# Performance work log

Measured on AMD Instinct MI355X. Metric: run time of the kernel, lower is better.

## Reference

```python
import math
import jax, jax.numpy as jnp
import numpy as np

H = 8      # num_heads
K = 3      # polynomial order
WH, WW = 8, 8  # win_size


def _relative_position_index(wh, ww):
    coords = np.stack(np.meshgrid(np.arange(wh), np.arange(ww), indexing='ij'))  # [2,wh,ww]
    cf = coords.reshape(2, -1)                       # [2, N]
    rel = cf[:, :, None] - cf[:, None, :]            # [2, N, N]
    rel = rel.transpose(1, 2, 0).astype(np.int64)    # [N, N, 2]
    rel[..., 0] += wh - 1
    rel[..., 1] += ww - 1
    rel[..., 0] *= 2 * ww - 1
    return rel.sum(-1)                               # [N, N]


def setup_inputs() -> dict:
    key = jax.random.key(0)
    ks = jax.random.split(key, 10)
    B, N, C = 1024, WH * WW, 256
    hd = C // H
    s = 0.02
    inp = {
        'x': jax.random.normal(ks[0], (B, N, C), dtype=jnp.float32),
        'Wq': jax.random.normal(ks[1], (C, C), dtype=jnp.float32) * s,
        'bq': jnp.zeros((C,), dtype=jnp.float32),
        'Wkv': jax.random.normal(ks[2], (C, 2 * C), dtype=jnp.float32) * s,
        'bkv': jnp.zeros((2 * C,), dtype=jnp.float32),
        'Wgate': jax.random.normal(ks[3], (hd, K + 1), dtype=jnp.float32) * s,
        'bgate': jnp.zeros((K + 1,), dtype=jnp.float32),
        'Wproj': jax.random.normal(ks[4], (C, C), dtype=jnp.float32) * s,
        'bproj': jnp.zeros((C,), dtype=jnp.float32),
        'bias_table': jax.random.normal(ks[5], ((2 * WH - 1) * (2 * WW - 1), H), dtype=jnp.float32) * s,
        'rel_index': jnp.asarray(_relative_position_index(WH, WW)),
    }
    return inp


def reference(x, Wq, bq, Wkv, bkv, Wgate, bgate, Wproj, bproj, bias_table, rel_index):
    B, N, C = x.shape
    hd = C // H
    # per-(batch,head) sigmoid gates over the K+1 polynomial orders
    gate = jax.nn.sigmoid(x.mean(axis=1).reshape(B, H, hd) @ Wgate + bgate)  # [B,H,K+1]
    gate = gate[..., None, None]                                             # [B,H,K+1,1,1]

    q = (x @ Wq + bq).reshape(B, N, H, hd).transpose(0, 2, 1, 3)             # [B,H,N,hd]
    kv = (x @ Wkv + bkv).reshape(B, N, 2, H, hd).transpose(2, 0, 3, 1, 4)
    k, v = kv[0], kv[1]                                                      # [B,H,N,hd]

    q = jax.nn.softmax(q, axis=-1)
    k = jax.nn.softmax(k, axis=-1)
    attn = jnp.einsum('bhnd,bhmd->bhnm', q, k)                               # [B,H,N,N] (>=0)

    bias = bias_table[rel_index.reshape(-1)].reshape(N, N, H).transpose(2, 0, 1)  # [H,N,N]
    attn = attn + jax.nn.relu(bias)[None]
    attn = (attn + attn.transpose(0, 1, 3, 2)) * 0.5

    # symmetric degree normalization: D^{-1/2} A D^{-1/2}, zero-degree rows untouched
    d = attn.sum(axis=-1)                                                    # [B,H,N]
    dn = jnp.where(d > 0, 1.0 / jnp.sqrt(jnp.where(d > 0, d, 1.0)), d)
    attn = attn * dn[:, :, None, :] * dn[:, :, :, None]

    I = jnp.eye(N, dtype=attn.dtype)
    L = I - attn        # Laplacian
    L_hat = I + attn    # 2I - L

    # tmp[i] = L_hat^i (tmp[0] = I broadcasts)
    tmp = [I]
    E = I
    for _ in range(K):
        E = E @ L_hat
        tmp.append(E)

    c = [math.comb(K, j) / 2 ** K for j in range(K + 1)]
    out = c[0] * gate[:, :, K] * (tmp[K] @ v)                                # [B,H,N,hd]
    E = I
    for j in range(K):
        E = E @ L
        out = out + c[j + 1] * gate[:, :, j] * (E @ (tmp[K - j - 1] @ v))

    out = out.transpose(0, 2, 1, 3).reshape(B, N, C)
    out = out @ Wproj + bproj
    return out
```

## Files before the change

### kernel.cpp

```cpp
#include <hip/hip_runtime.h>
#include <hip/hip_bf16.h>

typedef __attribute__((ext_vector_type(8))) short bf16x8;
typedef __attribute__((ext_vector_type(4))) float f32x4;

__device__ __forceinline__ unsigned short f2bf(float f) {
    union { __hip_bfloat16 h; unsigned short u; } c;
    c.h = __float2bfloat16(f);
    return c.u;
}
__device__ __forceinline__ unsigned int pk2(float lo, float hi) {
    return (unsigned int)f2bf(lo) | ((unsigned int)f2bf(hi) << 16);
}
__device__ __forceinline__ bf16x8 as_bf(uint4 u) {
    union { uint4 a; bf16x8 b; } c; c.a = u; return c.b;
}
__device__ __forceinline__ float bf2f(unsigned short us) {
    return __uint_as_float(((unsigned int)us) << 16);
}
__device__ __forceinline__ void gload_lds16(const void* g, void* l) {
    __builtin_amdgcn_global_load_lds(
        (const __attribute__((address_space(1))) void*)g,
        (__attribute__((address_space(3))) void*)l, 16, 0, 0);
}

__global__ __launch_bounds__(256) void prep_kernel(
    const float* __restrict__ x,
    const float* __restrict__ Wq, const float* __restrict__ Wkv, const float* __restrict__ Wproj,
    const float* __restrict__ Wgate, const float* __restrict__ bgate,
    const float* __restrict__ bias_table, const int* __restrict__ rel_index,
    unsigned short* __restrict__ xbf, int use_xbf,
    unsigned short* __restrict__ wq, unsigned short* __restrict__ wk,
    unsigned short* __restrict__ wv, unsigned short* __restrict__ wp,
    float* __restrict__ bsym, float* __restrict__ wpoly)
{
    const int bid = blockIdx.x, t = threadIdx.x;
    if (bid < 1024) {
        __shared__ float mean_s[256];
        __shared__ float gsig[32];
        const float* xb = x + (size_t)bid * 16384;
        float s = 0.f;
        if (use_xbf) {
            unsigned short* xo = xbf + (size_t)bid * 16384;
            #pragma unroll 4
            for (int n = 0; n < 64; n++) { float v = xb[n * 256 + t]; s += v; xo[n * 256 + t] = f2bf(v); }
        } else {
            #pragma unroll 8
            for (int n = 0; n < 64; n++) s += xb[n * 256 + t];
        }
        mean_s[t] = s * (1.f / 64.f);
        __syncthreads();
        if (t < 32) {
            int h = t >> 2, j = t & 3;
            float g = bgate[j];
            #pragma unroll 8
            for (int dd = 0; dd < 32; dd++) g = fmaf(mean_s[h * 32 + dd], Wgate[dd * 4 + j], g);
            gsig[t] = 1.f / (1.f + __expf(-g));
        }
        __syncthreads();
        if (t < 8) {
            float g0 = gsig[t * 4], g1 = gsig[t * 4 + 1], g2 = gsig[t * 4 + 2], g3 = gsig[t * 4 + 3];
            float a = 0.125f * g3, bb = 0.375f * g0, cc = 0.375f * g1, dd = 0.125f * g2;
            float4 o;
            o.x = a + bb + cc + dd;
            o.y = 3.f * a + bb - cc - 3.f * dd;
            o.z = 3.f * a - bb - cc + 3.f * dd;
            o.w = a - bb + cc - dd;
            ((float4*)wpoly)[bid * 8 + t] = o;
        }
    } else if (bid < 2048) {
        int e = (bid - 1024) * 256 + t;
        int m = e >> 16, r = e & 65535, o = r >> 8, kk = r & 255;
        float v; unsigned short* dst;
        if (m == 0)      { v = Wq[kk * 256 + o];        dst = wq; }
        else if (m == 1) { v = Wkv[kk * 512 + o];       dst = wk; }
        else if (m == 2) { v = Wkv[kk * 512 + 256 + o]; dst = wv; }
        else             { v = Wproj[kk * 256 + o];     dst = wp; }
        dst[o * 256 + kk] = f2bf(v);
    } else {
        int e = (bid - 2048) * 256 + t;
        int hh = e >> 12, ij = e & 4095;
        int i = ij >> 6, j = ij & 63;
        float bij = bias_table[rel_index[ij] * 8 + hh];
        float bji = bias_table[rel_index[j * 64 + i] * 8 + hh];
        bsym[hh * 4096 + ij] = 0.5f * (fmaxf(bij, 0.f) + fmaxf(bji, 0.f));
    }
}

template <bool XBF>
__global__ __launch_bounds__(256, 4) void attn_kernel(
    const float* __restrict__ x, const unsigned short* __restrict__ xbf,
    const float* __restrict__ bq, const float* __restrict__ bkv,
    const unsigned short* __restrict__ wq, const unsigned short* __restrict__ wk,
    const unsigned short* __restrict__ wv,
    const float* __restrict__ bsym, const float* __restrict__ wpoly,
    unsigned short* __restrict__ hid)
{
    __shared__ __align__(16) unsigned char tile[32768];
    float* dn = (float*)(tile + 28672);

    const int bid = blockIdx.x;
    const int xcd = bid & 7, idx = bid >> 3;
    const int b = xcd * 128 + (idx >> 3), h = idx & 7;
    const int t = threadIdx.x;
    const int l = t & 63, w = t >> 6;
    const int lr = l & 15, qg = l >> 4;

    const float4 wv4 = ((const float4*)wpoly)[b * 8 + h];

    const int role = w;
    uint4 Bfr0[8], Bfr1[8];
    {
        const unsigned short* wsel = (role == 0) ? wq : (role == 1) ? wk : wv;
        const uint4* Wp = (const uint4*)wsel;
        const int ct0 = (role < 2) ? 0 : (role - 2);
        const int o0 = h * 32 + ct0 * 16 + lr;
        #pragma unroll
        for (int ks = 0; ks < 8; ks++) Bfr0[ks] = Wp[o0 * 32 + ks * 4 + qg];
        if (role < 2) {
            #pragma unroll
            for (int ks = 0; ks < 8; ks++) Bfr1[ks] = Wp[(o0 + 16) * 32 + ks * 4 + qg];
        }
    }

    if (XBF) {
        const unsigned short* xb = xbf + (size_t)b * 16384;
        const int rp = l >> 5, u = l & 31;
        #pragma unroll
        for (int i = 0; i < 8; i++) {
            int row = i * 8 + w * 2 + rp;
            int csrc = (u & 24) | ((u & 7) ^ (row & 7));
            gload_lds16(xb + row * 256 + csrc * 8, tile + (i * 8 + w * 2) * 512);
        }
    } else {
        const float* xb = x + (size_t)b * 16384;
        #pragma unroll
        for (int i = 0; i < 8; i++) {
            int e = t + i * 256;
            int row = e >> 5, c = e & 31;
            const float4* p = (const float4*)(xb + row * 256 + c * 8);
            float4 f0 = p[0], f1 = p[1];
            uint4 u;
            u.x = pk2(f0.x, f0.y); u.y = pk2(f0.z, f0.w);
            u.z = pk2(f1.x, f1.y); u.w = pk2(f1.z, f1.w);
            *(uint4*)(tile + row * 512 + ((c >> 3) << 7) + (((c & 7) ^ (row & 7)) << 4)) = u;
        }
    }

    f32x4 acc0[4], acc1[4];
    {
        const int ct0 = (role < 2) ? 0 : (role - 2);
        const int o0 = h * 32 + ct0 * 16 + lr;
        float b0 = (role == 0) ? bq[o0] : (role == 1) ? bkv[o0] : bkv[256 + o0];
        float b1 = (role == 0) ? bq[o0 + 16] : (role == 1) ? bkv[o0 + 16] : 0.f;
        #pragma unroll
        for (int mt = 0; mt < 4; mt++) {
            f32x4 z0 = {b0, b0, b0, b0}; acc0[mt] = z0;
            f32x4 z1 = {b1, b1, b1, b1}; acc1[mt] = z1;
        }
    }
    __syncthreads();

    __builtin_amdgcn_s_setprio(1);
    if (role < 2) {
        #pragma unroll
        for (int mt = 0; mt < 4; mt++) {
            const int rowA = mt * 16 + lr;
            #pragma unroll
            for (int ks = 0; ks < 8; ks++) {
                const int c = ks * 4 + qg;
                bf16x8 af = *(const bf16x8*)(tile + rowA * 512 + ((c >> 3) << 7) + (((c & 7) ^ (rowA & 7)) << 4));
                acc0[mt] = __builtin_amdgcn_mfma_f32_16x16x32_bf16(af, as_bf(Bfr0[ks]), acc0[mt], 0, 0, 0);
                acc1[mt] = __builtin_amdgcn_mfma_f32_16x16x32_bf16(af, as_bf(Bfr1[ks]), acc1[mt], 0, 0, 0);
            }
        }
    } else {
        #pragma unroll
        for (int mt = 0; mt < 4; mt++) {
            const int rowA = mt * 16 + lr;
            #pragma unroll
            for (int ks = 0; ks < 8; ks++) {
                const int c = ks * 4 + qg;
                bf16x8 af = *(const bf16x8*)(tile + rowA * 512 + ((c >> 3) << 7) + (((c & 7) ^ (rowA & 7)) << 4));
                acc0[mt] = __builtin_amdgcn_mfma_f32_16x16x32_bf16(af, as_bf(Bfr0[ks]), acc0[mt], 0, 0, 0);
            }
        }
    }
    __builtin_amdgcn_s_setprio(0);
    __syncthreads();

    float bsv[4][4];
    {
        const float* bh_ = bsym + h * 4096;
        #pragma unroll
        for (int jt = 0; jt < 4; jt++)
            #pragma unroll
            for (int r = 0; r < 4; r++)
                bsv[jt][r] = bh_[(w * 16 + qg * 4 + r) * 64 + jt * 16 + lr];
    }

    if (role < 2) {
        #pragma unroll
        for (int mt = 0; mt < 4; mt++)
            #pragma unroll
            for (int r = 0; r < 4; r++) {
                float e0 = __expf(acc0[mt][r]), e1 = __expf(acc1[mt][r]);
                float s = e0 + e1;
                s += __shfl_xor(s, 1); s += __shfl_xor(s, 2);
                s += __shfl_xor(s, 4); s += __shfl_xor(s, 8);
                float inv = 1.f / s;
                acc0[mt][r] = e0 * inv; acc1[mt][r] = e1 * inv;
            }
    }

    if (role == 0) {
        #pragma unroll
        for (int mt = 0; mt < 4; mt++)
            #pragma unroll
            for (int r = 0; r < 4; r++) {
                int row = mt * 16 + qg * 4 + r;
                int d0 = lr, d1 = 16 + lr;
                *(short*)(tile + row * 128 + (((d0 >> 3) ^ (row & 7)) << 4) + (d0 & 7) * 2) = (short)f2bf(acc0[mt][r]);
                *(short*)(tile + row * 128 + (((d1 >> 3) ^ (row & 7)) << 4) + (d1 & 7) * 2) = (short)f2bf(acc1[mt][r]);
            }
    } else if (role == 1) {
        #pragma unroll
        for (int mt = 0; mt < 4; mt++)
            #pragma unroll
            for (int r = 0; r < 4; r++) {
                int row = mt * 16 + qg * 4 + r;
                int d0 = lr, d1 = 16 + lr;
                *(short*)(tile + 8192 + row * 128 + (((d0 >> 3) ^ (row & 7)) << 4) + (d0 & 7) * 2) = (short)f2bf(acc0[mt][r]);
                *(short*)(tile + 8192 + row * 128 + (((d1 >> 3) ^ (row & 7)) << 4) + (d1 & 7) * 2) = (short)f2bf(acc1[mt][r]);
            }
    } else {
        const int d = (role - 2) * 16 + lr;
        #pragma unroll
        for (int mt = 0; mt < 4; mt++)
            #pragma unroll
            for (int r = 0; r < 4; r++) {
                int row = mt * 16 + qg * 4 + r;
                *(short*)(tile + 16384 + d * 128 + (((row >> 3) ^ (d & 7)) << 4) + (row & 7) * 2) = (short)f2bf(acc0[mt][r]);
            }
    }
    __syncthreads();

    float sv[4][4];
    float dnv[4];
    {
        const int swz = (qg ^ (lr & 7)) << 4;
        bf16x8 aqf = *(const bf16x8*)(tile + (w * 16 + lr) * 128 + swz);
        bf16x8 akf = *(const bf16x8*)(tile + 8192 + (w * 16 + lr) * 128 + swz);
        float rs[4] = {0.f, 0.f, 0.f, 0.f};
        __builtin_amdgcn_s_setprio(1);
        #pragma unroll
        for (int jt = 0; jt < 4; jt++) {
            bf16x8 bqf = *(const bf16x8*)(tile + (jt * 16 + lr) * 128 + swz);
            bf16x8 bkf = *(const bf16x8*)(tile + 8192 + (jt * 16 + lr) * 128 + swz);
            f32x4 qk = {0.f, 0.f, 0.f, 0.f}, kq = {0.f, 0.f, 0.f, 0.f};
            qk = __builtin_amdgcn_mfma_f32_16x16x32_bf16(aqf, bkf, qk, 0, 0, 0);
            kq = __builtin_amdgcn_mfma_f32_16x16x32_bf16(akf, bqf, kq, 0, 0, 0);
            #pragma unroll
            for (int r = 0; r < 4; r++) {
                float v = 0.5f * (qk[r] + kq[r]) + bsv[jt][r];
                sv[jt][r] = v;
                rs[r] += v;
            }
        }
        __builtin_amdgcn_s_setprio(0);
        #pragma unroll
        for (int r = 0; r < 4; r++) {
            float s = rs[r];
            s += __shfl_xor(s, 1); s += __shfl_xor(s, 2);
            s += __shfl_xor(s, 4); s += __shfl_xor(s, 8);
            dnv[r] = (s > 0.f) ? rsqrtf(s) : s;
        }
        if (lr == 0) {
            int base = w * 16 + qg * 4;
            dn[base + 0] = dnv[0]; dn[base + 1] = dnv[1];
            dn[base + 2] = dnv[2]; dn[base + 3] = dnv[3];
        }
    }
    __syncthreads();

    const float w0c = wv4.x, w1c = wv4.y, w2c = wv4.z, w3c = wv4.w;
    f32x4 y[2];
    #pragma unroll
    for (int ct = 0; ct < 2; ct++)
        #pragma unroll
        for (int r = 0; r < 4; r++) {
            int row = w * 16 + qg * 4 + r;
            int d = ct * 16 + lr;
            unsigned short us = *(unsigned short*)(tile + 16384 + d * 128 + (((row >> 3) ^ (d & 7)) << 4) + (row & 7) * 2);
            y[ct][r] = w0c * bf2f(us);
        }

    {
        float dnj[4];
        #pragma unroll
        for (int jt = 0; jt < 4; jt++) dnj[jt] = dn[jt * 16 + lr];
        #pragma unroll
        for (int jt = 0; jt < 4; jt++)
            #pragma unroll
            for (int r = 0; r < 4; r++) {
                int i = w * 16 + qg * 4 + r, j = jt * 16 + lr;
                *(short*)(tile + i * 128 + (((j >> 3) ^ (i & 7)) << 4) + (j & 7) * 2)
                    = (short)f2bf(sv[jt][r] * dnv[r] * dnj[jt]);
            }
    }

#define AU_ROUND(SRC, DST, WC, WRITE) {                                                          \
    f32x4 u0 = {0.f,0.f,0.f,0.f}, u1 = {0.f,0.f,0.f,0.f};                                        \
    __builtin_amdgcn_s_setprio(1);                                                               \
    _Pragma("unroll")                                                                            \
    for (int ks2 = 0; ks2 < 2; ks2++) {                                                          \
        int c = ks2 * 4 + qg;                                                                    \
        bf16x8 af = *(const bf16x8*)(tile + (w * 16 + lr) * 128 + ((c ^ (lr & 7)) << 4));        \
        bf16x8 b0 = *(const bf16x8*)(tile + (SRC) + lr * 128 + ((c ^ (lr & 7)) << 4));           \
        bf16x8 b1 = *(const bf16x8*)(tile + (SRC) + (16 + lr) * 128 + ((c ^ (lr & 7)) << 4));    \
        u0 = __builtin_amdgcn_mfma_f32_16x16x32_bf16(af, b0, u0, 0, 0, 0);                       \
        u1 = __builtin_amdgcn_mfma_f32_16x16x32_bf16(af, b1, u1, 0, 0, 0);                       \
    }                                                                                            \
    __builtin_amdgcn_s_setprio(0);                                                               \
    y[0] += (WC) * u0; y[1] += (WC) * u1;                                                        \
    if (WRITE) {                                                                                 \
        _Pragma("unroll")                                                                        \
        for (int r = 0; r < 4; r++) {                                                            \
            int i = w * 16 + qg * 4 + r;                                                         \
            *(short*)(tile + (DST) + lr * 128 + (((i >> 3) ^ (lr & 7)) << 4) + (i & 7) * 2) = (short)f2bf(u0[r]); \
            *(short*)(tile + (DST) + (16 + lr) * 128 + (((i >> 3) ^ (lr & 7)) << 4) + (i & 7) * 2) = (short)f2bf(u1[r]); \
        }                                                                                        \
        __syncthreads();                                                                         \
    }                                                                                            \
}
    AU_ROUND(16384, 20480, w1c, 1)
    AU_ROUND(20480, 24576, w2c, 1)
    AU_ROUND(24576, 0,     w3c, 0)
#undef AU_ROUND

    #pragma unroll
    for (int ct = 0; ct < 2; ct++)
        #pragma unroll
        for (int r = 0; r < 4; r++) {
            int row = w * 16 + qg * 4 + r;
            int col = h * 32 + ct * 16 + lr;
            hid[((size_t)b * 64 + row) * 256 + col] = f2bf(y[ct][r]);
        }
}

__global__ __launch_bounds__(256) void proj_kernel(
    const unsigned short* __restrict__ hidden,
    const unsigned short* __restrict__ wp,
    const float* __restrict__ bproj,
    float* __restrict__ out)
{
    __shared__ __align__(16) unsigned char atile[65536];
    const int rb = blockIdx.x;
    const int t = threadIdx.x, l = t & 63, w = t >> 6;
    const int lr = l & 15, qg = l >> 4;

    const unsigned short* hb = hidden + (size_t)rb * 128 * 256;
    {
        const int rp = l >> 5, u = l & 31;
        #pragma unroll
        for (int i = 0; i < 16; i++) {
            int row = i * 8 + w * 2 + rp;
            int csrc = (u & 24) | ((u & 7) ^ (row & 7));
            gload_lds16(hb + row * 256 + csrc * 8, atile + (i * 8 + w * 2) * 512);
        }
    }
    float bzv[16];
    #pragma unroll
    for (int ct = 0; ct < 16; ct++) bzv[ct] = bproj[ct * 16 + lr];
    __syncthreads();

    bf16x8 af[2][8];
    #pragma unroll
    for (int rt = 0; rt < 2; rt++) {
        int row = w * 32 + rt * 16 + lr;
        #pragma unroll
        for (int ks = 0; ks < 8; ks++) {
            int c = ks * 4 + qg;
            af[rt][ks] = *(const bf16x8*)(atile + row * 512 + (((c & 24) | ((c & 7) ^ (row & 7))) << 4));
        }
    }

    const uint4* WP = (const uint4*)wp;
    #pragma unroll 2
    for (int ct = 0; ct < 16; ct++) {
        f32x4 a0 = {0.f, 0.f, 0.f, 0.f}, a1 = {0.f, 0.f, 0.f, 0.f};
        #pragma unroll
        for (int ks = 0; ks < 8; ks++) {
            bf16x8 bf = as_bf(WP[(ct * 16 + lr) * 32 + ks * 4 + qg]);
            a0 = __builtin_amdgcn_mfma_f32_16x16x32_bf16(af[0][ks], bf, a0, 0, 0, 0);
            a1 = __builtin_amdgcn_mfma_f32_16x16x32_bf16(af[1][ks], bf, a1, 0, 0, 0);
        }
        int colg = ct * 16 + lr;
        float bz = bzv[ct];
        #pragma unroll
        for (int r = 0; r < 4; r++) {
            int rowg = rb * 128 + w * 32 + qg * 4 + r;
            out[(size_t)rowg * 256 + colg] = a0[r] + bz;
            out[(size_t)(rowg + 16) * 256 + colg] = a1[r] + bz;
        }
    }
}

extern "C" void kernel_launch(void* const* d_in, const int* in_sizes, int n_in,
                              void* d_out, int out_size, void* d_ws, size_t ws_size,
                              hipStream_t stream) {
    const float* x          = (const float*)d_in[0];
    const float* Wq         = (const float*)d_in[1];
    const float* bq         = (const float*)d_in[2];
    const float* Wkv        = (const float*)d_in[3];
    const float* bkv        = (const float*)d_in[4];
    const float* Wgate      = (const float*)d_in[5];
    const float* bgate      = (const float*)d_in[6];
    const float* Wproj      = (const float*)d_in[7];
    const float* bproj      = (const float*)d_in[8];
    const float* bias_table = (const float*)d_in[9];
    const int*   rel_index  = (const int*)d_in[10];
    float* out = (float*)d_out;
    unsigned char* wsb = (unsigned char*)d_ws;

    const size_t HID   = 0;
    const size_t WQo   = 33554432;
    const size_t WKo   = WQo + 131072;
    const size_t WVo   = WKo + 131072;
    const size_t WPo   = WVo + 131072;
    const size_t BIASo = WPo + 131072;
    const size_t WPOLY = BIASo + 131072;
    const size_t XBFo  = WPOLY + 131072;
    const int use_xbf  = (ws_size >= XBFo + 33554432ull) ? 1 : 0;

    unsigned short* hid = (unsigned short*)(wsb + HID);
    unsigned short* wq  = (unsigned short*)(wsb + WQo);
    unsigned short* wk  = (unsigned short*)(wsb + WKo);
    unsigned short* wv  = (unsigned short*)(wsb + WVo);
    unsigned short* wp  = (unsigned short*)(wsb + WPo);
    float* bsym  = (float*)(wsb + BIASo);
    float* wpoly = (float*)(wsb + WPOLY);
    unsigned short* xbf = (unsigned short*)(wsb + XBFo);

    prep_kernel<<<dim3(2176), dim3(256), 0, stream>>>(
        x, Wq, Wkv, Wproj, Wgate, bgate, bias_table, rel_index,
        xbf, use_xbf, wq, wk, wv, wp, bsym, wpoly);
    if (use_xbf)
        attn_kernel<true><<<dim3(8192), dim3(256), 0, stream>>>(
            x, xbf, bq, bkv, wq, wk, wv, bsym, wpoly, hid);
    else
        attn_kernel<false><<<dim3(8192), dim3(256), 0, stream>>>(
            x, xbf, bq, bkv, wq, wk, wv, bsym, wpoly, hid);
    proj_kernel<<<dim3(512), dim3(256), 0, stream>>>(hid, wp, bproj, out);
}
```

Measured before the change: 141.3 us.

## Fuse gate computation into attention kernel and drop bf16 x pre-pass

Removes the prep-kernel pass that read all of x to compute per-batch means, sigmoid gates and a bf16 copy of x. The attention kernel now always loads fp32 x and converts it in registers, then computes the per-head column mean from the bf16 tile already in LDS and evaluates the gate with wave shuffles, sharing the coefficients through LDS. This avoids one full read of x plus the bf16 write and later re-read. In exchange, each block loads fp32 x instead of using async LDS loads of bf16, and the gate mean is now taken over bf16-rounded values, which slightly changes precision.

```diff
diff --git a/kernel.cpp b/kernel.cpp
--- a/kernel.cpp
+++ b/kernel.cpp
@@ -25,51 +25,15 @@
 }
 
 __global__ __launch_bounds__(256) void prep_kernel(
-    const float* __restrict__ x,
     const float* __restrict__ Wq, const float* __restrict__ Wkv, const float* __restrict__ Wproj,
-    const float* __restrict__ Wgate, const float* __restrict__ bgate,
     const float* __restrict__ bias_table, const int* __restrict__ rel_index,
-    unsigned short* __restrict__ xbf, int use_xbf,
     unsigned short* __restrict__ wq, unsigned short* __restrict__ wk,
     unsigned short* __restrict__ wv, unsigned short* __restrict__ wp,
-    float* __restrict__ bsym, float* __restrict__ wpoly)
+    float* __restrict__ bsym)
 {
     const int bid = blockIdx.x, t = threadIdx.x;
     if (bid < 1024) {
-        __shared__ float mean_s[256];
-        __shared__ float gsig[32];
-        const float* xb = x + (size_t)bid * 16384;
-        float s = 0.f;
-        if (use_xbf) {
-            unsigned short* xo = xbf + (size_t)bid * 16384;
-            #pragma unroll 4
-            for (int n = 0; n < 64; n++) { float v = xb[n * 256 + t]; s += v; xo[n * 256 + t] = f2bf(v); }
-        } else {
-            #pragma unroll 8
-            for (int n = 0; n < 64; n++) s += xb[n * 256 + t];
-        }
-        mean_s[t] = s * (1.f / 64.f);
-        __syncthreads();
-        if (t < 32) {
-            int h = t >> 2, j = t & 3;
-            float g = bgate[j];
-            #pragma unroll 8
-            for (int dd = 0; dd < 32; dd++) g = fmaf(mean_s[h * 32 + dd], Wgate[dd * 4 + j], g);
-            gsig[t] = 1.f / (1.f + __expf(-g));
-        }
-        __syncthreads();
-        if (t < 8) {
-            float g0 = gsig[t * 4], g1 = gsig[t * 4 + 1], g2 = gsig[t * 4 + 2], g3 = gsig[t * 4 + 3];
-            float a = 0.125f * g3, bb = 0.375f * g0, cc = 0.375f * g1, dd = 0.125f * g2;
-            float4 o;
-            o.x = a + bb + cc + dd;
-            o.y = 3.f * a + bb - cc - 3.f * dd;
-            o.z = 3.f * a - bb - cc + 3.f * dd;
-            o.w = a - bb + cc - dd;
-            ((float4*)wpoly)[bid * 8 + t] = o;
-        }
-    } else if (bid < 2048) {
-        int e = (bid - 1024) * 256 + t;
+        int e = bid * 256 + t;
         int m = e >> 16, r = e & 65535, o = r >> 8, kk = r & 255;
         float v; unsigned short* dst;
         if (m == 0)      { v = Wq[kk * 256 + o];        dst = wq; }
@@ -78,7 +42,7 @@
         else             { v = Wproj[kk * 256 + o];     dst = wp; }
         dst[o * 256 + kk] = f2bf(v);
     } else {
-        int e = (bid - 2048) * 256 + t;
+        int e = (bid - 1024) * 256 + t;
         int hh = e >> 12, ij = e & 4095;
         int i = ij >> 6, j = ij & 63;
         float bij = bias_table[rel_index[ij] * 8 + hh];
@@ -87,13 +51,13 @@
     }
 }
 
-template <bool XBF>
 __global__ __launch_bounds__(256, 4) void attn_kernel(
-    const float* __restrict__ x, const unsigned short* __restrict__ xbf,
+    const float* __restrict__ x,
     const float* __restrict__ bq, const float* __restrict__ bkv,
     const unsigned short* __restrict__ wq, const unsigned short* __restrict__ wk,
     const unsigned short* __restrict__ wv,
-    const float* __restrict__ bsym, const float* __restrict__ wpoly,
+    const float* __restrict__ bsym,
+    const float* __restrict__ Wgate, const float* __restrict__ bgate,
     unsigned short* __restrict__ hid)
 {
     __shared__ __align__(16) unsigned char tile[32768];
@@ -106,8 +70,6 @@
     const int l = t & 63, w = t >> 6;
     const int lr = l & 15, qg = l >> 4;
 
-    const float4 wv4 = ((const float4*)wpoly)[b * 8 + h];
-
     const int role = w;
     uint4 Bfr0[8], Bfr1[8];
     {
@@ -123,16 +85,7 @@
         }
     }
 
-    if (XBF) {
-        const unsigned short* xb = xbf + (size_t)b * 16384;
-        const int rp = l >> 5, u = l & 31;
-        #pragma unroll
-        for (int i = 0; i < 8; i++) {
-            int row = i * 8 + w * 2 + rp;
-            int csrc = (u & 24) | ((u & 7) ^ (row & 7));
-            gload_lds16(xb + row * 256 + csrc * 8, tile + (i * 8 + w * 2) * 512);
-        }
-    } else {
+    {
         const float* xb = x + (size_t)b * 16384;
         #pragma unroll
         for (int i = 0; i < 8; i++) {
@@ -187,7 +140,41 @@
         }
     }
     __builtin_amdgcn_s_setprio(0);
+
+    float g4[4];
+    if (role == 2) {
+        const int d = l & 31, rh = (l >> 5) * 32;
+        const int gcol = h * 32 + d;
+        const int cc = gcol >> 3;
+        const int eb = (gcol & 7) * 2;
+        float s = 0.f;
+        #pragma unroll
+        for (int r2 = 0; r2 < 32; r2++) {
+            int row = rh + r2;
+            s += bf2f(*(const unsigned short*)(tile + row * 512 + ((cc >> 3) << 7) + (((cc & 7) ^ (row & 7)) << 4) + eb));
+        }
+        s += __shfl_xor(s, 32);
+        float mean = s * (1.f / 64.f);
+        #pragma unroll
+        for (int j = 0; j < 4; j++) {
+            float p = mean * Wgate[d * 4 + j];
+            p += __shfl_xor(p, 1); p += __shfl_xor(p, 2);
+            p += __shfl_xor(p, 4); p += __shfl_xor(p, 8);
+            p += __shfl_xor(p, 16);
+            g4[j] = 1.f / (1.f + __expf(-(p + bgate[j])));
+        }
+    }
     __syncthreads();
+
+    if (role == 2 && l == 0) {
+        float a = 0.125f * g4[3], bb = 0.375f * g4[0], cc2 = 0.375f * g4[1], dd = 0.125f * g4[2];
+        float4 o;
+        o.x = a + bb + cc2 + dd;
+        o.y = 3.f * a + bb - cc2 - 3.f * dd;
+        o.z = 3.f * a - bb - cc2 + 3.f * dd;
+        o.w = a - bb + cc2 - dd;
+        *(float4*)(tile + 28928) = o;
+    }
 
     float bsv[4][4];
     {
@@ -244,6 +231,8 @@
             }
     }
     __syncthreads();
+
+    const float4 wv4 = *(const float4*)(tile + 28928);
 
     float sv[4][4];
     float dnv[4];
@@ -429,27 +418,17 @@
     const size_t WVo   = WKo + 131072;
     const size_t WPo   = WVo + 131072;
     const size_t BIASo = WPo + 131072;
-    const size_t WPOLY = BIASo + 131072;
-    const size_t XBFo  = WPOLY + 131072;
-    const int use_xbf  = (ws_size >= XBFo + 33554432ull) ? 1 : 0;
 
     unsigned short* hid = (unsigned short*)(wsb + HID);
     unsigned short* wq  = (unsigned short*)(wsb + WQo);
     unsigned short* wk  = (unsigned short*)(wsb + WKo);
     unsigned short* wv  = (unsigned short*)(wsb + WVo);
     unsigned short* wp  = (unsigned short*)(wsb + WPo);
-    float* bsym  = (float*)(wsb + BIASo);
-    float* wpoly = (float*)(wsb + WPOLY);
-    unsigned short* xbf = (unsigned short*)(wsb + XBFo);
-
-    prep_kernel<<<dim3(2176), dim3(256), 0, stream>>>(
-        x, Wq, Wkv, Wproj, Wgate, bgate, bias_table, rel_index,
-        xbf, use_xbf, wq, wk, wv, wp, bsym, wpoly);
-    if (use_xbf)
-        attn_kernel<true><<<dim3(8192), dim3(256), 0, stream>>>(
-            x, xbf, bq, bkv, wq, wk, wv, bsym, wpoly, hid);
-    else
-        attn_kernel<false><<<dim3(8192), dim3(256), 0, stream>>>(
-            x, xbf, bq, bkv, wq, wk, wv, bsym, wpoly, hid);
+    float* bsym = (float*)(wsb + BIASo);
+
+    prep_kernel<<<dim3(1152), dim3(256), 0, stream>>>(
+        Wq, Wkv, Wproj, bias_table, rel_index, wq, wk, wv, wp, bsym);
+    attn_kernel<<<dim3(8192), dim3(256), 0, stream>>>(
+        x, bq, bkv, wq, wk, wv, bsym, Wgate, bgate, hid);
     proj_kernel<<<dim3(512), dim3(256), 0, stream>>>(hid, wp, bproj, out);
 }
```

Measured after the change: 161.5 us. +14.3%, slower.
